# Performance work log

Hardware: AMD Instinct MI355X
Metric: run time of the kernel (lower is better)

The kernel has to match this reference:

```python
import jax, jax.numpy as jnp
import numpy as np

INPUTDIM = 256
OUTDIM = 64
GRIDSIZE = 300
BATCH = 2048


def setup_inputs() -> dict:
    key = jax.random.key(0)
    kx, kw = jax.random.split(key)
    x = jax.random.normal(kx, (BATCH, INPUTDIM), dtype=jnp.float32)
    stddev = 1.0 / (np.sqrt(INPUTDIM) * np.sqrt(GRIDSIZE))
    fouriercoeffs = jax.random.normal(kw, (2, OUTDIM, INPUTDIM, GRIDSIZE), dtype=jnp.float32) * stddev
    return {"x": x, "fouriercoeffs": fouriercoeffs}


def reference(x, fouriercoeffs):
    # k: frequencies 1..gridsize, shape [gridsize]
    gridsize = fouriercoeffs.shape[-1]
    k = jnp.arange(1, gridsize + 1, dtype=x.dtype)
    # phase [batch, inputdim, gridsize]
    phase = x[:, :, None] * k[None, None, :]
    c = jnp.cos(phase)
    s = jnp.sin(phase)
    # y[b,j] = sum_{i,k} c[b,i,k]*Wc[j,i,k] + s[b,i,k]*Ws[j,i,k]
    y = jnp.einsum('bik,jik->bj', c, fouriercoeffs[0]) + jnp.einsum('bik,jik->bj', s, fouriercoeffs[1])
    return y
```

## Files before the change

### kernel.cpp

```cpp
#include <hip/hip_runtime.h>
#include <hip/hip_bf16.h>

#define BATCH 2048
#define IDIM  256
#define ODIM  64
#define GRIDN 300

typedef __bf16 bf16x8 __attribute__((ext_vector_type(8)));
typedef float  f32x16 __attribute__((ext_vector_type(16)));
typedef float  f32x2  __attribute__((ext_vector_type(2)));
typedef unsigned int uint4v __attribute__((ext_vector_type(4)));

#define AS1 __attribute__((address_space(1)))
#define AS3 __attribute__((address_space(3)))

__device__ __forceinline__ unsigned short f2bf(float f) {
    return __builtin_bit_cast(unsigned short, __float2bfloat16(f));
}

__global__ __launch_bounds__(256) void fkan_prep(const float* __restrict__ fc,
                                                 char* __restrict__ wp) {
    __shared__ alignas(16) char lds[32768];
    const int blk = blockIdx.x;
    const int ib  = blk & 15;
    const int gb  = blk >> 4;
    const int g0  = gb * 8;
    const int G   = (gb == 37) ? 4 : 8;
    const int q   = threadIdx.x >> 6;
    const int j   = threadIdx.x & 63;

    float vals[2][4][8];
    #pragma unroll
    for (int t = 0; t < 2; ++t) {
        #pragma unroll
        for (int e = 0; e < 4; ++e) {
            const float* src = fc + (((size_t)t * ODIM + j) * IDIM
                                     + (ib * 16 + q * 4 + e)) * GRIDN + g0;
            float4 lo = *(const float4*)(src);
            vals[t][e][0] = lo.x; vals[t][e][1] = lo.y;
            vals[t][e][2] = lo.z; vals[t][e][3] = lo.w;
            if (G == 8) {
                float4 hi = *(const float4*)(src + 4);
                vals[t][e][4] = hi.x; vals[t][e][5] = hi.y;
                vals[t][e][6] = hi.z; vals[t][e][7] = hi.w;
            }
        }
    }
    #pragma unroll
    for (int g = 0; g < 8; ++g) {
        if (g < 4 || G == 8) {
            uint4v dw;
            #pragma unroll
            for (int e = 0; e < 4; ++e)
                dw[e] = (unsigned)f2bf(vals[0][e][g]) | ((unsigned)f2bf(vals[1][e][g]) << 16);
            *(uint4v*)(lds + g * 4096 + q * 1024 + j * 16) = dw;
        }
    }
    __syncthreads();
    char* dst = wp + ((size_t)ib * GRIDN + g0) * 4096;
    for (int w = threadIdx.x * 16; w < G * 4096; w += 256 * 16)
        *(uint4v*)(dst + w) = *(const uint4v*)(lds + w);
}

__global__ __launch_bounds__(256, 4) void fkan_main(const float* __restrict__ x,
                                                    const char* __restrict__ wp,
                                                    float* __restrict__ out) {
    __shared__ alignas(16) char lds[2][12288];

    const int bid    = blockIdx.x;
    const int xcd    = bid & 7;
    const int within = bid >> 3;
    const int slice  = xcd * 8 + (within & 7);
    const int mtile  = within >> 3;
    const int isplit = slice >> 2;
    const int gq     = slice & 3;
    const int g_begin = gq * 75;

    const int tid  = threadIdx.x;
    const int wave = tid >> 6;
    const int lane = tid & 63;
    const int l31  = lane & 31;
    const int kgrp = lane >> 5;
    const int row  = mtile * 128 + wave * 32 + l31;

    f32x2 vc[4], vs[4], vbc[4], vbs[4];
    const float* xrow = x + (size_t)row * IDIM + isplit * 16;
    #pragma unroll
    for (int h = 0; h < 2; ++h) {
        const float4 xv4 = *(const float4*)(xrow + h * 8 + kgrp * 4);
        float xa[4] = {xv4.x, xv4.y, xv4.z, xv4.w};
        #pragma unroll
        for (int p = 0; p < 4; ++p) {
            const int ss = h * 4 + p;
            const float xv = xa[p];
            float sb, cb;
            __sincosf(xv, &sb, &cb);
            vbc[ss >> 1][ss & 1] = cb; vbs[ss >> 1][ss & 1] = sb;
            float s0 = sb, c0 = cb;
            if (g_begin != 0) __sincosf((float)(g_begin + 1) * xv, &s0, &c0);
            vc[ss >> 1][ss & 1] = c0; vs[ss >> 1][ss & 1] = s0;
        }
    }

    const unsigned aq = (unsigned)kgrp * 1024 + (unsigned)l31 * 16;
    const char* wbase = wp + ((size_t)(isplit * GRIDN + g_begin)) * 4096 + tid * 16;

    #pragma unroll
    for (int p = 0; p < 3; ++p)
        __builtin_amdgcn_global_load_lds(
            (const AS1 unsigned int*)(wbase + (size_t)p * 4096),
            (AS3 unsigned int*)(&lds[0][0] + p * 4096 + tid * 16), 16, 0, 0);
    __syncthreads();

    f32x16 acc0 = {0,0,0,0,0,0,0,0,0,0,0,0,0,0,0,0};
    f32x16 acc1 = {0,0,0,0,0,0,0,0,0,0,0,0,0,0,0,0};

    for (int it = 0; it < 25; ++it) {
        const int cur = it & 1;
        if (it + 1 < 25) {
            #pragma unroll
            for (int p = 0; p < 3; ++p)
                __builtin_amdgcn_global_load_lds(
                    (const AS1 unsigned int*)(wbase + ((size_t)(it + 1) * 3 + p) * 4096),
                    (AS3 unsigned int*)(&lds[cur ^ 1][0] + p * 4096 + tid * 16),
                    16, 0, 0);
        }
        #pragma unroll
        for (int g = 0; g < 3; ++g) {
            const char* base = &lds[cur][0] + g * 4096;
            const bf16x8 b00 = *(const bf16x8*)(base + aq);
            const bf16x8 b01 = *(const bf16x8*)(base + aq + 512);
            const bf16x8 b10 = *(const bf16x8*)(base + aq + 2048);
            const bf16x8 b11 = *(const bf16x8*)(base + aq + 2560);
            uint4v a1, a2;
            #pragma unroll
            for (int p = 0; p < 4; ++p) {
                a1[p] = (unsigned)f2bf(vc[p >> 1][p & 1])
                      | ((unsigned)f2bf(vs[p >> 1][p & 1]) << 16);
                a2[p] = (unsigned)f2bf(vc[(4 + p) >> 1][p & 1])
                      | ((unsigned)f2bf(vs[(4 + p) >> 1][p & 1]) << 16);
            }
            const bf16x8 af1 = __builtin_bit_cast(bf16x8, a1);
            const bf16x8 af2 = __builtin_bit_cast(bf16x8, a2);
            __builtin_amdgcn_s_setprio(1);
            acc0 = __builtin_amdgcn_mfma_f32_32x32x16_bf16(af1, b00, acc0, 0, 0, 0);
            acc1 = __builtin_amdgcn_mfma_f32_32x32x16_bf16(af1, b01, acc1, 0, 0, 0);
            acc0 = __builtin_amdgcn_mfma_f32_32x32x16_bf16(af2, b10, acc0, 0, 0, 0);
            acc1 = __builtin_amdgcn_mfma_f32_32x32x16_bf16(af2, b11, acc1, 0, 0, 0);
            __builtin_amdgcn_s_setprio(0);
            #pragma unroll
            for (int qq = 0; qq < 4; ++qq) {
                const f32x2 c = vc[qq], s = vs[qq];
                vc[qq] = c * vbc[qq] - s * vbs[qq];
                vs[qq] = s * vbc[qq] + c * vbs[qq];
            }
        }
        __syncthreads();
    }

    #pragma unroll
    for (int r = 0; r < 16; ++r) {
        const int orow = mtile * 128 + wave * 32 + (r & 3) + 8 * (r >> 2) + 4 * kgrp;
        unsafeAtomicAdd(out + (size_t)orow * ODIM + l31, acc0[r]);
        unsafeAtomicAdd(out + (size_t)orow * ODIM + 32 + l31, acc1[r]);
    }
}

__global__ __launch_bounds__(256) void fkan_naive(const float* __restrict__ x,
                                                  const float* __restrict__ fc,
                                                  float* __restrict__ out) {
    const int j = blockIdx.x >> 3;
    const int b = (blockIdx.x & 7) * 256 + threadIdx.x;
    const float* xr = x + (size_t)b * IDIM;
    float acc = 0.f;
    for (int i = 0; i < IDIM; ++i) {
        const float xv = xr[i];
        float sb, cb;
        __sincosf(xv, &sb, &cb);
        float c = cb, s = sb;
        const float* wc = fc + ((size_t)j * IDIM + i) * GRIDN;
        const float* ws = wc + (size_t)ODIM * IDIM * GRIDN;
        for (int g = 0; g < GRIDN; ++g) {
            acc += c * wc[g] + s * ws[g];
            const float cn = c * cb - s * sb;
            s = s * cb + c * sb;
            c = cn;
        }
    }
    out[(size_t)b * ODIM + j] = acc;
}

extern "C" void kernel_launch(void* const* d_in, const int* in_sizes, int n_in,
                              void* d_out, int out_size, void* d_ws, size_t ws_size,
                              hipStream_t stream) {
    const float* x  = (const float*)d_in[0];
    const float* fc = (const float*)d_in[1];
    float* out = (float*)d_out;
    constexpr size_t WPB = 16ull * GRIDN * 4096;

    if (ws_size >= WPB) {
        hipMemsetAsync(d_out, 0, (size_t)out_size * sizeof(float), stream);
        fkan_prep<<<608, 256, 0, stream>>>(fc, (char*)d_ws);
        fkan_main<<<1024, 256, 0, stream>>>(x, (const char*)d_ws, out);
    } else {
        fkan_naive<<<512, 256, 0, stream>>>(x, fc, out);
    }
}
```

Measured before the change: 85.72 us.

## Give each wave two 32-row M tiles to reuse B fragments, halve block size

Blocks shrink to two waves, and each wave now covers 64 batch rows instead of 32. Every B fragment read from LDS feeds two MFMAs, which halves the LDS read traffic per MFMA, and the weight tile per block is split across six 2KB loads. The fp32-to-bf16 packing also switches to inline v_cvt_pk_bf16_f32 asm. The cost is double the accumulators and sin/cos state per thread, so register pressure rises and occupancy may fall, and there are half as many waves per block to hide latency.

Result: no change. 86.04 us (+0.4%).

```diff
diff --git a/kernel.cpp b/kernel.cpp
--- a/kernel.cpp
+++ b/kernel.cpp
@@ -62,9 +62,9 @@
         *(uint4v*)(dst + w) = *(const uint4v*)(lds + w);
 }
 
-__global__ __launch_bounds__(256, 4) void fkan_main(const float* __restrict__ x,
-                                                    const char* __restrict__ wp,
-                                                    float* __restrict__ out) {
+__global__ __launch_bounds__(128) void fkan_main(const float* __restrict__ x,
+                                                 const char* __restrict__ wp,
+                                                 float* __restrict__ out) {
     __shared__ alignas(16) char lds[2][12288];
 
     const int bid    = blockIdx.x;
@@ -81,24 +81,27 @@
     const int lane = tid & 63;
     const int l31  = lane & 31;
     const int kgrp = lane >> 5;
-    const int row  = mtile * 128 + wave * 32 + l31;
-
-    f32x2 vc[4], vs[4], vbc[4], vbs[4];
-    const float* xrow = x + (size_t)row * IDIM + isplit * 16;
-    #pragma unroll
-    for (int h = 0; h < 2; ++h) {
-        const float4 xv4 = *(const float4*)(xrow + h * 8 + kgrp * 4);
-        float xa[4] = {xv4.x, xv4.y, xv4.z, xv4.w};
+    const int rowbase = mtile * 128 + wave * 64;
+
+    f32x2 vc[8], vs[8], vbc[8], vbs[8];
+    #pragma unroll
+    for (int rh = 0; rh < 2; ++rh) {
+        const float* xrow = x + (size_t)(rowbase + rh * 32 + l31) * IDIM + isplit * 16;
         #pragma unroll
-        for (int p = 0; p < 4; ++p) {
-            const int ss = h * 4 + p;
-            const float xv = xa[p];
-            float sb, cb;
-            __sincosf(xv, &sb, &cb);
-            vbc[ss >> 1][ss & 1] = cb; vbs[ss >> 1][ss & 1] = sb;
-            float s0 = sb, c0 = cb;
-            if (g_begin != 0) __sincosf((float)(g_begin + 1) * xv, &s0, &c0);
-            vc[ss >> 1][ss & 1] = c0; vs[ss >> 1][ss & 1] = s0;
+        for (int ih = 0; ih < 2; ++ih) {
+            const float4 xv4 = *(const float4*)(xrow + ih * 8 + kgrp * 4);
+            float xa[4] = {xv4.x, xv4.y, xv4.z, xv4.w};
+            #pragma unroll
+            for (int p = 0; p < 4; ++p) {
+                const int q = rh * 4 + ih * 2 + (p >> 1);
+                const float xv = xa[p];
+                float sb, cb;
+                __sincosf(xv, &sb, &cb);
+                vbc[q][p & 1] = cb; vbs[q][p & 1] = sb;
+                float s0 = sb, c0 = cb;
+                if (g_begin != 0) __sincosf((float)(g_begin + 1) * xv, &s0, &c0);
+                vc[q][p & 1] = c0; vs[q][p & 1] = s0;
+            }
         }
     }
 
@@ -106,23 +109,25 @@
     const char* wbase = wp + ((size_t)(isplit * GRIDN + g_begin)) * 4096 + tid * 16;
 
     #pragma unroll
-    for (int p = 0; p < 3; ++p)
+    for (int p = 0; p < 6; ++p)
         __builtin_amdgcn_global_load_lds(
-            (const AS1 unsigned int*)(wbase + (size_t)p * 4096),
-            (AS3 unsigned int*)(&lds[0][0] + p * 4096 + tid * 16), 16, 0, 0);
+            (const AS1 unsigned int*)(wbase + (size_t)p * 2048),
+            (AS3 unsigned int*)(&lds[0][0] + p * 2048 + tid * 16), 16, 0, 0);
     __syncthreads();
 
-    f32x16 acc0 = {0,0,0,0,0,0,0,0,0,0,0,0,0,0,0,0};
-    f32x16 acc1 = {0,0,0,0,0,0,0,0,0,0,0,0,0,0,0,0};
+    f32x16 acc00 = {0,0,0,0,0,0,0,0,0,0,0,0,0,0,0,0};
+    f32x16 acc01 = {0,0,0,0,0,0,0,0,0,0,0,0,0,0,0,0};
+    f32x16 acc10 = {0,0,0,0,0,0,0,0,0,0,0,0,0,0,0,0};
+    f32x16 acc11 = {0,0,0,0,0,0,0,0,0,0,0,0,0,0,0,0};
 
     for (int it = 0; it < 25; ++it) {
         const int cur = it & 1;
         if (it + 1 < 25) {
             #pragma unroll
-            for (int p = 0; p < 3; ++p)
+            for (int p = 0; p < 6; ++p)
                 __builtin_amdgcn_global_load_lds(
-                    (const AS1 unsigned int*)(wbase + ((size_t)(it + 1) * 3 + p) * 4096),
-                    (AS3 unsigned int*)(&lds[cur ^ 1][0] + p * 4096 + tid * 16),
+                    (const AS1 unsigned int*)(wbase + ((size_t)(it + 1) * 6 + p) * 2048),
+                    (AS3 unsigned int*)(&lds[cur ^ 1][0] + p * 2048 + tid * 16),
                     16, 0, 0);
         }
         #pragma unroll
@@ -132,27 +137,42 @@
             const bf16x8 b01 = *(const bf16x8*)(base + aq + 512);
             const bf16x8 b10 = *(const bf16x8*)(base + aq + 2048);
             const bf16x8 b11 = *(const bf16x8*)(base + aq + 2560);
-            uint4v a1, a2;
+            uint4v a00, a01, a10, a11;
             #pragma unroll
             for (int p = 0; p < 4; ++p) {
-                a1[p] = (unsigned)f2bf(vc[p >> 1][p & 1])
-                      | ((unsigned)f2bf(vs[p >> 1][p & 1]) << 16);
-                a2[p] = (unsigned)f2bf(vc[(4 + p) >> 1][p & 1])
-                      | ((unsigned)f2bf(vs[(4 + p) >> 1][p & 1]) << 16);
-            }
-            const bf16x8 af1 = __builtin_bit_cast(bf16x8, a1);
-            const bf16x8 af2 = __builtin_bit_cast(bf16x8, a2);
+                unsigned r;
+                asm("v_cvt_pk_bf16_f32 %0, %1, %2" : "=v"(r)
+                    : "v"(vc[(p >> 1)][p & 1]),     "v"(vs[(p >> 1)][p & 1]));
+                a00[p] = r;
+                asm("v_cvt_pk_bf16_f32 %0, %1, %2" : "=v"(r)
+                    : "v"(vc[2 + (p >> 1)][p & 1]), "v"(vs[2 + (p >> 1)][p & 1]));
+                a01[p] = r;
+                asm("v_cvt_pk_bf16_f32 %0, %1, %2" : "=v"(r)
+                    : "v"(vc[4 + (p >> 1)][p & 1]), "v"(vs[4 + (p >> 1)][p & 1]));
+                a10[p] = r;
+                asm("v_cvt_pk_bf16_f32 %0, %1, %2" : "=v"(r)
+                    : "v"(vc[6 + (p >> 1)][p & 1]), "v"(vs[6 + (p >> 1)][p & 1]));
+                a11[p] = r;
+            }
+            const bf16x8 af00 = __builtin_bit_cast(bf16x8, a00);
+            const bf16x8 af01 = __builtin_bit_cast(bf16x8, a01);
+            const bf16x8 af10 = __builtin_bit_cast(bf16x8, a10);
+            const bf16x8 af11 = __builtin_bit_cast(bf16x8, a11);
             __builtin_amdgcn_s_setprio(1);
-            acc0 = __builtin_amdgcn_mfma_f32_32x32x16_bf16(af1, b00, acc0, 0, 0, 0);
-            acc1 = __builtin_amdgcn_mfma_f32_32x32x16_bf16(af1, b01, acc1, 0, 0, 0);
-            acc0 = __builtin_amdgcn_mfma_f32_32x32x16_bf16(af2, b10, acc0, 0, 0, 0);
-            acc1 = __builtin_amdgcn_mfma_f32_32x32x16_bf16(af2, b11, acc1, 0, 0, 0);
+            acc00 = __builtin_amdgcn_mfma_f32_32x32x16_bf16(af00, b00, acc00, 0, 0, 0);
+            acc01 = __builtin_amdgcn_mfma_f32_32x32x16_bf16(af00, b01, acc01, 0, 0, 0);
+            acc10 = __builtin_amdgcn_mfma_f32_32x32x16_bf16(af10, b00, acc10, 0, 0, 0);
+            acc11 = __builtin_amdgcn_mfma_f32_32x32x16_bf16(af10, b01, acc11, 0, 0, 0);
+            acc00 = __builtin_amdgcn_mfma_f32_32x32x16_bf16(af01, b10, acc00, 0, 0, 0);
+            acc01 = __builtin_amdgcn_mfma_f32_32x32x16_bf16(af01, b11, acc01, 0, 0, 0);
+            acc10 = __builtin_amdgcn_mfma_f32_32x32x16_bf16(af11, b10, acc10, 0, 0, 0);
+            acc11 = __builtin_amdgcn_mfma_f32_32x32x16_bf16(af11, b11, acc11, 0, 0, 0);
             __builtin_amdgcn_s_setprio(0);
             #pragma unroll
-            for (int qq = 0; qq < 4; ++qq) {
-                const f32x2 c = vc[qq], s = vs[qq];
-                vc[qq] = c * vbc[qq] - s * vbs[qq];
-                vs[qq] = s * vbc[qq] + c * vbs[qq];
+            for (int q = 0; q < 8; ++q) {
+                const f32x2 c = vc[q], s = vs[q];
+                vc[q] = c * vbc[q] - s * vbs[q];
+                vs[q] = s * vbc[q] + c * vbs[q];
             }
         }
         __syncthreads();
@@ -160,9 +180,13 @@
 
     #pragma unroll
     for (int r = 0; r < 16; ++r) {
-        const int orow = mtile * 128 + wave * 32 + (r & 3) + 8 * (r >> 2) + 4 * kgrp;
-        unsafeAtomicAdd(out + (size_t)orow * ODIM + l31, acc0[r]);
-        unsafeAtomicAdd(out + (size_t)orow * ODIM + 32 + l31, acc1[r]);
+        const int rbase = (r & 3) + 8 * (r >> 2) + 4 * kgrp;
+        const int orow0 = rowbase + rbase;
+        const int orow1 = rowbase + 32 + rbase;
+        unsafeAtomicAdd(out + (size_t)orow0 * ODIM + l31,      acc00[r]);
+        unsafeAtomicAdd(out + (size_t)orow0 * ODIM + 32 + l31, acc01[r]);
+        unsafeAtomicAdd(out + (size_t)orow1 * ODIM + l31,      acc10[r]);
+        unsafeAtomicAdd(out + (size_t)orow1 * ODIM + 32 + l31, acc11[r]);
     }
 }
 
@@ -201,7 +225,7 @@
     if (ws_size >= WPB) {
         hipMemsetAsync(d_out, 0, (size_t)out_size * sizeof(float), stream);
         fkan_prep<<<608, 256, 0, stream>>>(fc, (char*)d_ws);
-        fkan_main<<<1024, 256, 0, stream>>>(x, (const char*)d_ws, out);
+        fkan_main<<<1024, 128, 0, stream>>>(x, (const char*)d_ws, out);
     } else {
         fkan_naive<<<512, 256, 0, stream>>>(x, fc, out);
     }
```
